# Kernel tuning notes

Hardware: AMD Instinct MI355X
Metric: run time of the kernel (lower is better)

Reference implementation:

```python
import jax, jax.numpy as jnp
import numpy as np

B, S, H, NH, HD, ROT = 4, 1024, 2048, 16, 128, 64
P = NH * HD  # attention projection size = 2048
EPS = 1e-6


def setup_inputs() -> dict:
    key = jax.random.key(0)
    ks = jax.random.split(key, 12)
    T = B * S
    # rotary frequency table [max_pos=S, 1, ROT]
    inv_freq = 1.0 / (10000.0 ** (np.arange(0, ROT, 2, dtype=np.float32) / ROT))
    f = np.outer(np.arange(S, dtype=np.float32), inv_freq)  # [S, ROT/2]
    freqs = np.concatenate([f, f], axis=-1)[:, None, :].astype(np.float32)
    sc = 0.02
    return {
        "positions": jnp.tile(jnp.arange(S, dtype=jnp.int64), B),  # per-seq positions 0..S-1
        "hidden_states": jax.random.normal(ks[0], (T, H), jnp.float32),
        "rotary_pos_emb": jnp.asarray(freqs),
        "lf1_cache": jax.random.normal(ks[1], (B, 1, H), jnp.float32) * sc,
        "lf2_cache": jax.random.normal(ks[2], (B, 1, H // 2), jnp.float32) * sc,
        "Wqk": jax.random.normal(ks[3], (2 * P, H), jnp.float32) * sc,
        "Wv": jax.random.normal(ks[4], (P, H), jnp.float32) * sc,
        "Wo": jax.random.normal(ks[5], (H, P), jnp.float32) * sc,
        "conv1_w": jax.random.normal(ks[6], (H // 2, H, 2), jnp.float32) * sc,  # [out, in, tap]
        "conv1_b": jnp.zeros((H // 2,), jnp.float32),
        "conv2_w": jax.random.normal(ks[7], (H, H // 2, 2), jnp.float32) * sc,
        "conv2_b": jnp.zeros((H,), jnp.float32),
        "ln_g": jnp.ones((H,), jnp.float32),
    }


def reference(positions, hidden_states, rotary_pos_emb, lf1_cache, lf2_cache,
              Wqk, Wv, Wo, conv1_w, conv1_b, conv2_w, conv2_b, ln_g):
    T = hidden_states.shape[0]
    scaling = HD ** -0.5

    # v projection on raw hidden states (done before lf_gate in the source)
    v = hidden_states @ Wv.T  # [T, P]

    # ---- LocalizedFiltering (two causal 2-tap convs + residual + RMSNorm),
    # vectorized over all sequences (source loops per sequence) ----
    x = hidden_states.reshape(B, S, H)
    xc = jnp.concatenate([lf1_cache, x], axis=1)  # [B, S+1, H]
    o1 = (jnp.einsum('bsh,oh->bso', xc[:, :-1], conv1_w[..., 0])
          + jnp.einsum('bsh,oh->bso', xc[:, 1:], conv1_w[..., 1]) + conv1_b)  # [B,S,H/2]
    o1c = jnp.concatenate([lf2_cache, o1], axis=1)  # [B, S+1, H/2]
    o2 = (jnp.einsum('bsc,oc->bso', o1c[:, :-1], conv2_w[..., 0])
          + jnp.einsum('bsc,oc->bso', o1c[:, 1:], conv2_w[..., 1]) + conv2_b)  # [B,S,H]
    o3 = o2 + x
    lf = o3 * jax.lax.rsqrt(jnp.mean(o3 * o3, axis=-1, keepdims=True) + EPS) * ln_g

    hs = lf.reshape(T, H)
    qk = (hs @ Wqk.T).reshape(T, NH, 2 * HD)
    q, k = jnp.split(qk, 2, axis=-1)  # each [T, NH, HD]

    # partial rotary (mscale = 1.0 since use_yarn=False)
    f = rotary_pos_emb[positions]            # [T, 1, ROT]
    cos, sin = jnp.cos(f), jnp.sin(f)

    def rope(t):
        tr, tp = t[..., :ROT], t[..., ROT:]
        t1, t2 = jnp.split(tr, 2, axis=-1)
        rot = jnp.concatenate([-t2, t1], axis=-1)
        return jnp.concatenate([tr * cos + rot * sin, tp], axis=-1)

    qb = rope(q).reshape(B, S, NH, HD)
    kb = rope(k).reshape(B, S, NH, HD)
    vb = v.reshape(B, S, NH, HD)

    # causal attention per sequence
    scores = jnp.einsum('bqhd,bkhd->bhqk', qb, kb) * scaling
    mask = jnp.tril(jnp.ones((S, S), bool))
    scores = jnp.where(mask, scores, jnp.finfo(scores.dtype).min)
    attn = jax.nn.softmax(scores, axis=-1)
    out = jnp.einsum('bhqk,bkhd->bqhd', attn, vb).reshape(T, P)
    return out @ Wo.T  # [T, H]
```

## Files before the change

### kernel.cpp

```cpp
#include <hip/hip_runtime.h>

typedef __bf16 bf16;
typedef __bf16 bf16x8 __attribute__((ext_vector_type(8)));
typedef __bf16 bf16x4 __attribute__((ext_vector_type(4)));
typedef float f32x4 __attribute__((ext_vector_type(4)));

#define DEVI __device__ __forceinline__

constexpr int Bc = 4, Sc = 1024, Hc = 2048, NHc = 16, HDc = 128;
constexpr int Tc = Bc * Sc;
constexpr int Pc = NHc * HDc;

DEVI void async16(const void* g, void* l) {
  __builtin_amdgcn_global_load_lds(
      (const __attribute__((address_space(1))) unsigned int*)g,
      (__attribute__((address_space(3))) unsigned int*)l, 16, 0, 0);
}

#define BAR() __builtin_amdgcn_s_barrier()
#define LGKM0()                                          \
  do {                                                   \
    asm volatile("s_waitcnt lgkmcnt(0)" ::: "memory");   \
    __builtin_amdgcn_sched_barrier(0);                   \
  } while (0)
#define VM0() asm volatile("s_waitcnt vmcnt(0)" ::: "memory")

template <int WM, int WN, int MREP, int NREP, bool OUT_BF16>
__global__ __launch_bounds__(512, 2) void gemm8(
    const bf16* __restrict__ A, const bf16* __restrict__ W, void* __restrict__ Cout,
    const float* __restrict__ bias, int M, int N, int K) {
  constexpr int BM = WM * MREP * 16;
  constexpr int BN = WN * NREP * 16;
  constexpr int MH = MREP / 2, NH = NREP / 2;
  constexpr int LA = BM / 128;
  constexpr int LB = BN / 128;
  constexpr int STG = (BM + BN) * 128;
  constexpr int OUTB = OUT_BF16 ? 2 : 4;
  constexpr int CBYTES = BM * BN * OUTB;
  constexpr int LDSB = (2 * STG > CBYTES) ? 2 * STG : CBYTES;
  __shared__ char lds[LDSB];

  const int nbx = N / BN;
  const int nwg = (M / BM) * nbx;
  const int wgid = (blockIdx.x & 7) * (nwg >> 3) + (blockIdx.x >> 3);
  const int bx = wgid % nbx, by = wgid / nbx;
  const int m0 = by * BM, n0 = bx * BN;
  const int tid = threadIdx.x;
  const int w = tid >> 6, l = tid & 63;
  const int wm = w / WN, wn = w % WN;
  const int lr = l & 15, hi = l >> 4;

  auto stageA = [&](int buf, int t, int half) {
#pragma unroll
    for (int c = 0; c < LA; ++c) {
      const int ch = c * 512 + tid;
      const int row = half * (BM / 2) + (ch >> 3);
      const int grp = ch & 7;
      async16(A + (size_t)(m0 + row) * K + (t << 6) + ((grp ^ (row & 7)) << 3),
              &lds[buf * STG + row * 128 + grp * 16]);
    }
  };
  auto stageB = [&](int buf, int t, int half) {
#pragma unroll
    for (int c = 0; c < LB; ++c) {
      const int ch = c * 512 + tid;
      const int row = half * (BN / 2) + (ch >> 3);
      const int grp = ch & 7;
      async16(W + (size_t)(n0 + row) * K + (t << 6) + ((grp ^ (row & 7)) << 3),
              &lds[buf * STG + BM * 128 + row * 128 + grp * 16]);
    }
  };
  auto LD = [&](const char* Lp, int row, int g) -> bf16x8 {
    return *(const bf16x8*)(Lp + ((size_t)row << 7) + ((g ^ (row & 7)) << 4));
  };

#define QUAD(MB_, NB_, FB_)                                                     \
  do {                                                                          \
    __builtin_amdgcn_s_setprio(1);                                              \
    _Pragma("unroll") for (int m = 0; m < MH; ++m)                              \
      _Pragma("unroll") for (int n = 0; n < NH; ++n)                            \
        _Pragma("unroll") for (int kk = 0; kk < 2; ++kk)                        \
          acc[(MB_) + m][(NB_) + n] = __builtin_amdgcn_mfma_f32_16x16x32_bf16(  \
              fa[m][kk], FB_[n][kk], acc[(MB_) + m][(NB_) + n], 0, 0, 0);       \
    __builtin_amdgcn_s_setprio(0);                                              \
  } while (0)

  f32x4 acc[MREP][NREP] = {};
  bf16x8 fa[MH][2], fb0[NH][2], fb1[NH][2];
  const int nk = K >> 6;

  stageA(0, 0, 0);
  stageB(0, 0, 0);
  stageB(0, 0, 1);
  stageA(0, 0, 1);
  VM0();
  BAR();

#pragma unroll 1
  for (int t = 0; t < nk; ++t) {
    const char* Lb = &lds[(t & 1) * STG];
    const int nbuf = (t & 1) ^ 1;
    const bool pf = (t + 1 < nk);
#pragma unroll
    for (int m = 0; m < MH; ++m) {
      const int r = wm * (MREP * 16) + m * 16 + lr;
      fa[m][0] = LD(Lb, r, hi);
      fa[m][1] = LD(Lb, r, 4 + hi);
    }
#pragma unroll
    for (int n = 0; n < NH; ++n) {
      const int r = BM + wn * (NREP * 16) + n * 16 + lr;
      fb0[n][0] = LD(Lb, r, hi);
      fb0[n][1] = LD(Lb, r, 4 + hi);
    }
    if (pf) {
      stageA(nbuf, t + 1, 0);
      stageB(nbuf, t + 1, 0);
    }
    BAR();
    LGKM0();
    QUAD(0, 0, fb0);
    BAR();
#pragma unroll
    for (int n = 0; n < NH; ++n) {
      const int r = BM + wn * (NREP * 16) + (NH + n) * 16 + lr;
      fb1[n][0] = LD(Lb, r, hi);
      fb1[n][1] = LD(Lb, r, 4 + hi);
    }
    if (pf) {
      stageB(nbuf, t + 1, 1);
      stageA(nbuf, t + 1, 1);
    }
    BAR();
    LGKM0();
    QUAD(0, NH, fb1);
    BAR();
#pragma unroll
    for (int m = 0; m < MH; ++m) {
      const int r = wm * (MREP * 16) + (MH + m) * 16 + lr;
      fa[m][0] = LD(Lb, r, hi);
      fa[m][1] = LD(Lb, r, 4 + hi);
    }
    BAR();
    LGKM0();
    QUAD(MH, NH, fb1);
    BAR();
    QUAD(MH, 0, fb0);
    VM0();
    BAR();
  }
#undef QUAD

  if constexpr (OUT_BF16) {
    bf16* cl = (bf16*)lds;
#pragma unroll
    for (int mi = 0; mi < MREP; ++mi) {
#pragma unroll
      for (int ni = 0; ni < NREP; ++ni) {
        const int col = wn * (NREP * 16) + ni * 16 + lr;
        const float bv = bias ? bias[n0 + col] : 0.f;
#pragma unroll
        for (int j = 0; j < 4; ++j) {
          const int row = wm * (MREP * 16) + mi * 16 + (hi << 2) + j;
          cl[row * BN + ((((col >> 3) ^ (row & 7)) << 3) | (col & 7))] =
              (bf16)(acc[mi][ni][j] + bv);
        }
      }
    }
    __syncthreads();
    constexpr int GPR = BN / 8;
    constexpr int PT = BM * GPR / 512;
#pragma unroll
    for (int c = 0; c < PT; ++c) {
      const int ch = c * 512 + tid;
      const int row = ch / GPR, g = ch % GPR;
      bf16x8 vv = *(const bf16x8*)&cl[row * BN + ((g ^ (row & 7)) << 3)];
      *(bf16x8*)&((bf16*)Cout)[(size_t)(m0 + row) * N + n0 + g * 8] = vv;
    }
  } else {
    float* cl = (float*)lds;
#pragma unroll
    for (int mi = 0; mi < MREP; ++mi) {
#pragma unroll
      for (int ni = 0; ni < NREP; ++ni) {
        const int col = wn * (NREP * 16) + ni * 16 + lr;
        const float bv = bias ? bias[n0 + col] : 0.f;
#pragma unroll
        for (int j = 0; j < 4; ++j) {
          const int row = wm * (MREP * 16) + mi * 16 + (hi << 2) + j;
          cl[row * BN + ((((col >> 2) ^ (row & 7)) << 2) | (col & 3))] =
              acc[mi][ni][j] + bv;
        }
      }
    }
    __syncthreads();
    constexpr int GPR = BN / 4;
    constexpr int PT = BM * GPR / 512;
#pragma unroll
    for (int c = 0; c < PT; ++c) {
      const int ch = c * 512 + tid;
      const int row = ch / GPR, g = ch % GPR;
      f32x4 vv = *(const f32x4*)&cl[row * BN + ((g ^ (row & 7)) << 2)];
      *(f32x4*)&((float*)Cout)[(size_t)(m0 + row) * N + n0 + g * 4] = vv;
    }
  }
}

template <int WM, int WN, int MREP, int NREP, bool OUT_BF16>
__global__ __launch_bounds__(WM * WN * 64, 2) void gemm_pipe(
    const bf16* __restrict__ A, const bf16* __restrict__ W, void* __restrict__ Cout,
    const float* __restrict__ bias, int M, int N, int K) {
  constexpr int BM = WM * MREP * 16;
  constexpr int BN = WN * NREP * 16;
  constexpr int THREADS = WM * WN * 64;
  constexpr int ROWS = BM + BN;
  constexpr int CHA = BM * 4 / THREADS;
  constexpr int CHB = BN * 4 / THREADS;
  static_assert(CHA + CHB == 4, "vmcnt ledger assumes 4 loads/thread/stage");
  __shared__ bf16 lds[4][ROWS * 32];
  static_assert(BM * BN * 2 <= sizeof(lds), "C tile must fit LDS for epilogue");

  const int nbx = N / BN;
  const int nwg = (M / BM) * nbx;
  const int wgid = (blockIdx.x & 7) * (nwg >> 3) + (blockIdx.x >> 3);
  const int bx = wgid % nbx, by = wgid / nbx;
  const int m0 = by * BM, n0 = bx * BN;
  const int tid = threadIdx.x;
  const int w = tid >> 6, l = tid & 63;
  const int wm = w / WN, wn = w % WN;
  const int lr = l & 15;
  const int hi = l >> 4;

  auto stage = [&](int slot, int t) {
    const int k0 = t << 5;
#pragma unroll
    for (int c = 0; c < CHA; ++c) {
      const int ch = c * THREADS + tid;
      const int row = ch >> 2, cg = ch & 3;
      const int gc = (cg ^ ((row >> 1) & 3)) << 3;
      async16(A + (size_t)(m0 + row) * K + k0 + gc, (char*)&lds[slot][0] + ch * 16);
    }
#pragma unroll
    for (int c = 0; c < CHB; ++c) {
      const int ch = c * THREADS + tid;
      const int row = ch >> 2, cg = ch & 3;
      const int gc = (cg ^ ((row >> 1) & 3)) << 3;
      async16(W + (size_t)(n0 + row) * K + k0 + gc,
              (char*)&lds[slot][0] + (BM * 4 + ch) * 16);
    }
  };

  f32x4 acc[MREP][NREP] = {};
  const int nk = K >> 5;

  stage(0, 0);
  stage(1, 1);
  stage(2, 2);
  asm volatile("s_waitcnt vmcnt(8)" ::: "memory");
  __builtin_amdgcn_s_barrier();
  __builtin_amdgcn_sched_barrier(0);

  bf16x8 fAc[MREP], fBc[NREP], fAn[MREP], fBn[NREP];
  {
    const char* nb = (const char*)&lds[0][0];
#pragma unroll
    for (int mi = 0; mi < MREP; ++mi) {
      const int r = wm * (MREP * 16) + mi * 16 + lr;
      fAc[mi] = *(const bf16x8*)(nb + r * 64 + ((hi ^ ((r >> 1) & 3)) << 4));
    }
#pragma unroll
    for (int ni = 0; ni < NREP; ++ni) {
      const int r = BM + wn * (NREP * 16) + ni * 16 + lr;
      fBc[ni] = *(const bf16x8*)(nb + r * 64 + ((hi ^ ((r >> 1) & 3)) << 4));
    }
  }

#define GSTEP(T_, CA, CB, NA, NB)                                              \
  do {                                                                         \
    if ((T_) + 2 < nk) asm volatile("s_waitcnt vmcnt(4)" ::: "memory");        \
    else               asm volatile("s_waitcnt vmcnt(0)" ::: "memory");        \
    __builtin_amdgcn_s_barrier();                                              \
    __builtin_amdgcn_sched_barrier(0);                                         \
    if ((T_) + 3 < nk) stage(((T_) + 3) & 3, (T_) + 3);                        \
    if ((T_) + 1 < nk) {                                                       \
      const char* nb = (const char*)&lds[((T_) + 1) & 3][0];                   \
      _Pragma("unroll") for (int mi = 0; mi < MREP; ++mi) {                    \
        const int r = wm * (MREP * 16) + mi * 16 + lr;                         \
        NA[mi] = *(const bf16x8*)(nb + r * 64 + ((hi ^ ((r >> 1) & 3)) << 4)); \
      }                                                                        \
      _Pragma("unroll") for (int ni = 0; ni < NREP; ++ni) {                    \
        const int r = BM + wn * (NREP * 16) + ni * 16 + lr;                    \
        NB[ni] = *(const bf16x8*)(nb + r * 64 + ((hi ^ ((r >> 1) & 3)) << 4)); \
      }                                                                        \
    }                                                                          \
    __builtin_amdgcn_s_setprio(1);                                             \
    _Pragma("unroll") for (int mi = 0; mi < MREP; ++mi)                        \
      _Pragma("unroll") for (int ni = 0; ni < NREP; ++ni)                      \
        acc[mi][ni] =                                                          \
            __builtin_amdgcn_mfma_f32_16x16x32_bf16(CA[mi], CB[ni], acc[mi][ni], 0, 0, 0); \
    __builtin_amdgcn_s_setprio(0);                                             \
  } while (0)

  for (int t = 0; t < nk; t += 2) {
    GSTEP(t, fAc, fBc, fAn, fBn);
    GSTEP(t + 1, fAn, fBn, fAc, fBc);
  }
#undef GSTEP

  __syncthreads();
  {
    bf16* cl = (bf16*)&lds[0][0];
#pragma unroll
    for (int mi = 0; mi < MREP; ++mi) {
#pragma unroll
      for (int ni = 0; ni < NREP; ++ni) {
        const int col = wn * (NREP * 16) + ni * 16 + lr;
        const float bv = bias ? bias[n0 + col] : 0.f;
#pragma unroll
        for (int j = 0; j < 4; ++j) {
          const int row = wm * (MREP * 16) + mi * 16 + (hi << 2) + j;
          cl[row * BN + ((((col >> 3) ^ (row & 7)) << 3) | (col & 7))] =
              (bf16)(acc[mi][ni][j] + bv);
        }
      }
    }
    __syncthreads();
    constexpr int GPR = BN / 8;
    constexpr int PT = BM * GPR / THREADS;
#pragma unroll
    for (int c = 0; c < PT; ++c) {
      const int ch = c * THREADS + tid;
      const int row = ch / GPR, g = ch % GPR;
      bf16x8 vv = *(const bf16x8*)&cl[row * BN + ((g ^ (row & 7)) << 3)];
      *(bf16x8*)&((bf16*)Cout)[(size_t)(m0 + row) * N + n0 + g * 8] = vv;
    }
  }
}

__global__ void k_f2b4(const float* __restrict__ in, bf16* __restrict__ out, int n4) {
  int i = blockIdx.x * 256 + threadIdx.x;
  if (i >= n4) return;
  float4 v = ((const float4*)in)[i];
  bf16x4 o = {(bf16)v.x, (bf16)v.y, (bf16)v.z, (bf16)v.w};
  ((bf16x4*)out)[i] = o;
}

__global__ void k_build_a1(const float* __restrict__ hid, const float* __restrict__ lf1,
                           bf16* __restrict__ hsb, bf16* __restrict__ A1) {
  int idx = blockIdx.x * 256 + threadIdx.x;
  int t = idx >> 11, h = idx & 2047;
  float x = hid[idx];
  hsb[idx] = (bf16)x;
  float xp;
  if ((t & (Sc - 1)) == 0)
    xp = lf1[(t >> 10) * Hc + h];
  else
    xp = hid[idx - Hc];
  size_t a = ((size_t)t << 12) + 2 * h;
  A1[a] = (bf16)xp;
  A1[a + 1] = (bf16)x;
}

__global__ void k_build_a2(const bf16* __restrict__ o1, const float* __restrict__ lf2,
                           bf16* __restrict__ A2) {
  int idx = blockIdx.x * 256 + threadIdx.x;
  int t = idx >> 10, c = idx & 1023;
  bf16 cur = o1[idx];
  bf16 prev;
  if ((t & (Sc - 1)) == 0)
    prev = (bf16)lf2[(t >> 10) * 1024 + c];
  else
    prev = o1[idx - 1024];
  size_t a = ((size_t)t << 11) + 2 * c;
  A2[a] = prev;
  A2[a + 1] = cur;
}

__global__ __launch_bounds__(256) void k_rmsnorm(const bf16* __restrict__ o2,
                                                 const float* __restrict__ hid,
                                                 const float* __restrict__ g,
                                                 bf16* __restrict__ lf) {
  int t = blockIdx.x, tid = threadIdx.x;
  size_t base = ((size_t)t << 11) + tid * 8;
  bf16x8 ov = *(const bf16x8*)&o2[base];
  const float* hp = &hid[base];
  float vals[8];
  float ss = 0.f;
#pragma unroll
  for (int i = 0; i < 8; ++i) {
    float x = (float)ov[i] + hp[i];
    vals[i] = x;
    ss += x * x;
  }
#pragma unroll
  for (int off = 1; off < 64; off <<= 1) ss += __shfl_xor(ss, off);
  __shared__ float red[4];
  if ((tid & 63) == 0) red[tid >> 6] = ss;
  __syncthreads();
  float tot = red[0] + red[1] + red[2] + red[3];
  float inv = rsqrtf(tot * (1.f / 2048.f) + 1e-6f);
  bf16x8 o;
#pragma unroll
  for (int i = 0; i < 8; ++i) o[i] = (bf16)(vals[i] * inv * g[tid * 8 + i]);
  *(bf16x8*)&lf[base] = o;
}

__global__ void k_rope(const bf16* __restrict__ qk, const float* __restrict__ rot,
                       bf16* __restrict__ qr, bf16* __restrict__ kr) {
  int bid = blockIdx.x;
  int n = bid & 15, t = bid >> 4;
  int s = t & (Sc - 1), b = t >> 10;
  int tid = threadIdx.x;
  int isk = tid >> 7, d = tid & 127;
  const bf16* src = qk + ((size_t)t << 12) + n * 256 + isk * 128;
  float val = (float)src[d];
  float outv = val;
  if (d < 64) {
    float f = rot[s * 64 + d];
    float c = cosf(f), sn = sinf(f);
    float other = (float)src[d ^ 32];
    outv = (d < 32) ? (val * c - other * sn) : (val * c + other * sn);
  }
  bf16* dst = isk ? kr : qr;
  dst[((size_t)((b * 16 + n) * 1024 + s) << 7) + d] = (bf16)outv;
}

__global__ void k_vt(const bf16* __restrict__ v, bf16* __restrict__ vT) {
  __shared__ bf16 tile[32][33];
  int bid = blockIdx.x;
  int dt = bid & 3;
  int st = (bid >> 2) & 31;
  int bn = bid >> 7;
  int b = bn >> 4, n = bn & 15;
  int tx = threadIdx.x & 31, ty = threadIdx.x >> 5;
#pragma unroll
  for (int i = 0; i < 4; ++i) {
    int s = st * 32 + ty + i * 8;
    int d = dt * 32 + tx;
    tile[ty + i * 8][tx] = v[(size_t)(b * 1024 + s) * 2048 + n * 128 + d];
  }
  __syncthreads();
#pragma unroll
  for (int i = 0; i < 4; ++i) {
    int d = dt * 32 + ty + i * 8;
    int s = st * 32 + tx;
    vT[((size_t)(bn * 128 + d)) * 1024 + s] = tile[tx][ty + i * 8];
  }
}

__global__ __launch_bounds__(256, 2) void k_attn(const bf16* __restrict__ qr,
                                                 const bf16* __restrict__ kr,
                                                 const bf16* __restrict__ vT,
                                                 bf16* __restrict__ att) {
  __shared__ bf16 Ks[2][64 * 128];
  __shared__ bf16 Vs[2][128 * 64];
  __shared__ bf16 plds[4][16 * 64];
  const int bid = blockIdx.x;
  const int xcd = bid & 7, jj = bid >> 3;
  const int bn = xcd * 8 + (jj >> 3);
  const int pr = jj & 7;
  const int tid = threadIdx.x, w = tid >> 6, l = tid & 63;
  const int lr = l & 15, hi = l >> 4;
  const bf16* kb = kr + ((size_t)bn << 17);
  const bf16* vb = vT + ((size_t)bn << 17);
  const int b = bn >> 4, hh = bn & 15;
  const float scaling = 0.08838834764831845f;

  auto stage = [&](int buf, int kt) {
#pragma unroll
    for (int c = 0; c < 4; ++c) {
      int chunk = c * 256 + tid;
      int prow = chunk >> 4, pcg = chunk & 15;
      async16(kb + ((size_t)(kt * 64 + prow) << 7) + ((pcg ^ (prow & 7)) << 3),
              (char*)&Ks[buf][0] + chunk * 16);
    }
#pragma unroll
    for (int c = 0; c < 4; ++c) {
      int chunk = c * 256 + tid;
      int prow = chunk >> 3, pcg = chunk & 7;
      async16(vb + ((size_t)prow << 10) + kt * 64 + ((pcg ^ (prow & 7)) << 3),
              (char*)&Vs[buf][0] + chunk * 16);
    }
  };

#pragma unroll 1
  for (int phase = 0; phase < 2; ++phase) {
    const int qt = phase ? (15 - pr) : pr;
    const int qg0 = qt * 64 + w * 16;
    const bf16* qb = qr + ((size_t)(bn * 1024 + qg0) << 7);
    bf16x8 qf[4];
#pragma unroll
    for (int ks = 0; ks < 4; ++ks) qf[ks] = *(const bf16x8*)&qb[lr * 128 + ks * 32 + hi * 8];
    f32x4 oacc[8] = {};
    float mrow[4] = {-1e30f, -1e30f, -1e30f, -1e30f};
    float lrow[4] = {0.f, 0.f, 0.f, 0.f};
    const int nkb = qt + 1;

    stage(0, 0);
    __syncthreads();

    for (int kbt = 0; kbt < nkb; ++kbt) {
      const int cur = kbt & 1;
      if (kbt + 1 < nkb) stage(cur ^ 1, kbt + 1);

      f32x4 sacc[4] = {};
#pragma unroll
      for (int n = 0; n < 4; ++n) {
        const int krow = n * 16 + lr;
#pragma unroll
        for (int ks = 0; ks < 4; ++ks) {
          bf16x8 kf = *(const bf16x8*)&Ks[cur][(krow << 7) + ((((ks << 2) | hi) ^ (krow & 7)) << 3)];
          sacc[n] = __builtin_amdgcn_mfma_f32_16x16x32_bf16(qf[ks], kf, sacc[n], 0, 0, 0);
        }
      }
      const bool needmask = (kbt * 64 + 63 > qg0);
#pragma unroll
      for (int n = 0; n < 4; ++n) {
        int kg = kbt * 64 + n * 16 + lr;
#pragma unroll
        for (int j = 0; j < 4; ++j) {
          float sv = sacc[n][j] * scaling;
          if (needmask && kg > qg0 + hi * 4 + j) sv = -1e30f;
          sacc[n][j] = sv;
        }
      }
      float sf[4];
#pragma unroll
      for (int j = 0; j < 4; ++j) {
        float pm = fmaxf(fmaxf(sacc[0][j], sacc[1][j]), fmaxf(sacc[2][j], sacc[3][j]));
        pm = fmaxf(pm, __shfl_xor(pm, 1));
        pm = fmaxf(pm, __shfl_xor(pm, 2));
        pm = fmaxf(pm, __shfl_xor(pm, 4));
        pm = fmaxf(pm, __shfl_xor(pm, 8));
        float mn = fmaxf(mrow[j], pm);
        sf[j] = __expf(mrow[j] - mn);
        mrow[j] = mn;
      }
#pragma unroll
      for (int n = 0; n < 4; ++n)
#pragma unroll
        for (int j = 0; j < 4; ++j) sacc[n][j] = __expf(sacc[n][j] - mrow[j]);
#pragma unroll
      for (int j = 0; j < 4; ++j) {
        float ps = sacc[0][j] + sacc[1][j] + sacc[2][j] + sacc[3][j];
        ps += __shfl_xor(ps, 1);
        ps += __shfl_xor(ps, 2);
        ps += __shfl_xor(ps, 4);
        ps += __shfl_xor(ps, 8);
        lrow[j] = lrow[j] * sf[j] + ps;
      }
#pragma unroll
      for (int dt = 0; dt < 8; ++dt)
#pragma unroll
        for (int j = 0; j < 4; ++j) oacc[dt][j] *= sf[j];
#pragma unroll
      for (int n = 0; n < 4; ++n)
#pragma unroll
        for (int j = 0; j < 4; ++j)
          plds[w][(hi * 4 + j) * 64 + n * 16 + lr] = (bf16)sacc[n][j];
      asm volatile("s_waitcnt lgkmcnt(0)" ::: "memory");
#pragma unroll
      for (int ks2 = 0; ks2 < 2; ++ks2) {
        bf16x8 pf = *(const bf16x8*)&plds[w][lr * 64 + ks2 * 32 + hi * 8];
#pragma unroll
        for (int dt = 0; dt < 8; ++dt) {
          const int vrow = dt * 16 + lr;
          bf16x8 vf = *(const bf16x8*)&Vs[cur][(vrow << 6) + ((((ks2 << 2) | hi) ^ (lr & 7)) << 3)];
          oacc[dt] = __builtin_amdgcn_mfma_f32_16x16x32_bf16(pf, vf, oacc[dt], 0, 0, 0);
        }
      }
      __syncthreads();
    }

#pragma unroll
    for (int j = 0; j < 4; ++j) {
      float inv = 1.f / lrow[j];
      int qg = qg0 + hi * 4 + j;
      size_t obase = ((size_t)(b * 1024 + qg) << 11) + hh * 128;
#pragma unroll
      for (int dt = 0; dt < 8; ++dt) att[obase + dt * 16 + lr] = (bf16)(oacc[dt][j] * inv);
    }
  }
}

extern "C" void kernel_launch(void* const* d_in, const int* in_sizes, int n_in,
                              void* d_out, int out_size, void* d_ws, size_t ws_size,
                              hipStream_t stream) {
  const float* hid = (const float*)d_in[1];
  const float* rot = (const float*)d_in[2];
  const float* lf1 = (const float*)d_in[3];
  const float* lf2 = (const float*)d_in[4];
  const float* Wqk = (const float*)d_in[5];
  const float* Wv  = (const float*)d_in[6];
  const float* Wo  = (const float*)d_in[7];
  const float* c1w = (const float*)d_in[8];
  const float* c1b = (const float*)d_in[9];
  const float* c2w = (const float*)d_in[10];
  const float* c2b = (const float*)d_in[11];
  const float* lng = (const float*)d_in[12];
  float* outp = (float*)d_out;
  char* ws = (char*)d_ws;

  const size_t MB = 1ull << 20;
  bf16* Wslot = (bf16*)(ws + 0 * MB);
  bf16* A1    = (bf16*)(ws + 16 * MB);
  bf16* qkb   = A1;
  bf16* hsb   = (bf16*)(ws + 48 * MB);
  bf16* lfb   = hsb;
  bf16* vT    = hsb;
  bf16* v     = (bf16*)(ws + 64 * MB);
  bf16* att   = v;
  bf16* o1    = (bf16*)(ws + 80 * MB);
  bf16* A2    = (bf16*)(ws + 88 * MB);
  bf16* qr    = A2;
  bf16* o2    = (bf16*)(ws + 104 * MB);
  bf16* kr    = o2;

  auto f2b = [&](const float* in, bf16* out, int n) {
    int n4 = n / 4;
    k_f2b4<<<(n4 + 255) / 256, 256, 0, stream>>>(in, out, n4);
  };

  f2b(Wv, Wslot, 2048 * 2048);
  k_build_a1<<<Tc * Hc / 256, 256, 0, stream>>>(hid, lf1, hsb, A1);
  gemm8<4, 2, 4, 4, true><<<256, 512, 0, stream>>>(hsb, Wslot, v, nullptr, Tc, Pc, Hc);

  f2b(c1w, Wslot, 1024 * 2048 * 2);
  gemm_pipe<2, 2, 4, 4, true><<<256, 256, 0, stream>>>(A1, Wslot, o1, c1b, Tc, 1024, 4096);

  k_build_a2<<<Tc * 1024 / 256, 256, 0, stream>>>(o1, lf2, A2);
  f2b(c2w, Wslot, 2048 * 1024 * 2);
  gemm8<4, 2, 4, 4, true><<<256, 512, 0, stream>>>(A2, Wslot, o2, c2b, Tc, 2048, 2048);

  k_rmsnorm<<<Tc, 256, 0, stream>>>(o2, hid, lng, lfb);

  f2b(Wqk, Wslot, 4096 * 2048);
  gemm8<2, 4, 8, 4, true><<<256, 512, 0, stream>>>(lfb, Wslot, qkb, nullptr, Tc, 4096, Hc);

  k_rope<<<Tc * NHc, 256, 0, stream>>>(qkb, rot, qr, kr);
  k_vt<<<64 * 32 * 4, 256, 0, stream>>>(v, vT);
  k_attn<<<Bc * NHc * 8, 256, 0, stream>>>(qr, kr, vT, att);

  f2b(Wo, Wslot, 2048 * 2048);
  gemm8<4, 2, 4, 4, false><<<256, 512, 0, stream>>>(att, Wslot, outp, nullptr, Tc, 2048, 2048);
}
```

Measured before the change: 389.9 us.

## Fuse RoPE and V-transpose into GEMM epilogues, drop separate kernels

The QK projection GEMM now applies partial rotary embedding in its epilogue and writes q and k directly in head-major layout. The V projection GEMM writes its tile transposed straight into the vT layout. This removes the separate k_rope and k_vt kernels along with their extra global read and write passes over qk and v, and two launches. In exchange the epilogues compute sin and cos per element and issue strided stores, and the workspace buffers are reassigned.

```diff
diff --git a/kernel.cpp b/kernel.cpp
--- a/kernel.cpp
+++ b/kernel.cpp
@@ -25,17 +25,19 @@
   } while (0)
 #define VM0() asm volatile("s_waitcnt vmcnt(0)" ::: "memory")
 
-template <int WM, int WN, int MREP, int NREP, bool OUT_BF16>
+template <int WM, int WN, int MREP, int NREP, int EPI>
 __global__ __launch_bounds__(512, 2) void gemm8(
-    const bf16* __restrict__ A, const bf16* __restrict__ W, void* __restrict__ Cout,
-    const float* __restrict__ bias, int M, int N, int K) {
+    const bf16* __restrict__ A, const bf16* __restrict__ W,
+    void* __restrict__ C0, void* __restrict__ C1,
+    const float* __restrict__ biasf, const float* __restrict__ rotf,
+    int M, int N, int K) {
   constexpr int BM = WM * MREP * 16;
   constexpr int BN = WN * NREP * 16;
   constexpr int MH = MREP / 2, NH = NREP / 2;
   constexpr int LA = BM / 128;
   constexpr int LB = BN / 128;
   constexpr int STG = (BM + BN) * 128;
-  constexpr int OUTB = OUT_BF16 ? 2 : 4;
+  constexpr int OUTB = (EPI == 3) ? 4 : 2;
   constexpr int CBYTES = BM * BN * OUTB;
   constexpr int LDSB = (2 * STG > CBYTES) ? 2 * STG : CBYTES;
   __shared__ char lds[LDSB];
@@ -151,14 +153,14 @@
   }
 #undef QUAD
 
-  if constexpr (OUT_BF16) {
+  if constexpr (EPI == 0) {
     bf16* cl = (bf16*)lds;
 #pragma unroll
-    for (int mi = 0; mi < MREP; ++mi) {
+    for (int mi = 0; mi < MREP; ++mi)
 #pragma unroll
       for (int ni = 0; ni < NREP; ++ni) {
         const int col = wn * (NREP * 16) + ni * 16 + lr;
-        const float bv = bias ? bias[n0 + col] : 0.f;
+        const float bv = biasf ? biasf[n0 + col] : 0.f;
 #pragma unroll
         for (int j = 0; j < 4; ++j) {
           const int row = wm * (MREP * 16) + mi * 16 + (hi << 2) + j;
@@ -166,7 +168,6 @@
               (bf16)(acc[mi][ni][j] + bv);
         }
       }
-    }
     __syncthreads();
     constexpr int GPR = BN / 8;
     constexpr int PT = BM * GPR / 512;
@@ -175,16 +176,88 @@
       const int ch = c * 512 + tid;
       const int row = ch / GPR, g = ch % GPR;
       bf16x8 vv = *(const bf16x8*)&cl[row * BN + ((g ^ (row & 7)) << 3)];
-      *(bf16x8*)&((bf16*)Cout)[(size_t)(m0 + row) * N + n0 + g * 8] = vv;
+      *(bf16x8*)&((bf16*)C0)[(size_t)(m0 + row) * N + n0 + g * 8] = vv;
+    }
+  } else if constexpr (EPI == 1) {
+    bf16* cl = (bf16*)lds;
+#pragma unroll
+    for (int mi = 0; mi < MREP; ++mi)
+#pragma unroll
+      for (int ni = 0; ni < NREP; ++ni) {
+        const int col = wn * (NREP * 16) + ni * 16 + lr;
+#pragma unroll
+        for (int j = 0; j < 4; ++j) {
+          const int row = wm * (MREP * 16) + mi * 16 + (hi << 2) + j;
+          cl[col * BM + ((((row >> 3) ^ (col & 7)) << 3) | (row & 7))] =
+              (bf16)acc[mi][ni][j];
+        }
+      }
+    __syncthreads();
+    const int s0 = m0 & 1023, bq = m0 >> 10;
+    bf16* vT = (bf16*)C0;
+    const size_t vbase = (((size_t)(bq * 16 + (n0 >> 7)) * 128) << 10) + s0;
+    constexpr int GPR = BM / 8;
+    constexpr int PT = BN * GPR / 512;
+#pragma unroll
+    for (int c = 0; c < PT; ++c) {
+      const int ch = c * 512 + tid;
+      const int d = ch / GPR, g = ch % GPR;
+      bf16x8 vv = *(const bf16x8*)&cl[d * BM + ((g ^ (d & 7)) << 3)];
+      *(bf16x8*)&vT[vbase + ((size_t)d << 10) + g * 8] = vv;
+    }
+  } else if constexpr (EPI == 2) {
+    bf16* cl = (bf16*)lds;
+#pragma unroll
+    for (int mi = 0; mi < MREP; ++mi)
+#pragma unroll
+      for (int ni = 0; ni < NREP; ++ni) {
+        const int col = wn * (NREP * 16) + ni * 16 + lr;
+#pragma unroll
+        for (int j = 0; j < 4; ++j) {
+          const int row = wm * (MREP * 16) + mi * 16 + (hi << 2) + j;
+          cl[row * BN + ((((col >> 3) ^ (row & 7)) << 3) | (col & 7))] =
+              (bf16)acc[mi][ni][j];
+        }
+      }
+    __syncthreads();
+    const int s0 = m0 & 1023, bq = m0 >> 10, head = n0 >> 8;
+    bf16* qr = (bf16*)C0;
+    bf16* kr = (bf16*)C1;
+    const size_t qbase = ((size_t)((bq * 16 + head) * 1024 + s0) << 7);
+    constexpr int GPR = BN / 8;
+    constexpr int PT = BM * GPR / 512;
+#pragma unroll
+    for (int c = 0; c < PT; ++c) {
+      const int ch = c * 512 + tid;
+      const int row = ch / GPR, g = ch % GPR;
+      const int cc = g * 8;
+      const int isk = cc >> 7, dd = cc & 127;
+      bf16x8 vv = *(const bf16x8*)&cl[row * BN + ((g ^ (row & 7)) << 3)];
+      bf16x8 out;
+      if (dd < 64) {
+        bf16x8 pp = *(const bf16x8*)&cl[row * BN + (((g ^ 4) ^ (row & 7)) << 3)];
+        const float* rp = &rotf[(s0 + row) * 64 + dd];
+#pragma unroll
+        for (int e = 0; e < 8; ++e) {
+          const float f = rp[e];
+          const float cf = cosf(f), sf = sinf(f);
+          const float pv = (dd < 32) ? -(float)pp[e] : (float)pp[e];
+          out[e] = (bf16)((float)vv[e] * cf + pv * sf);
+        }
+      } else {
+        out = vv;
+      }
+      bf16* dst = isk ? kr : qr;
+      *(bf16x8*)&dst[qbase + ((size_t)row << 7) + dd] = out;
     }
   } else {
     float* cl = (float*)lds;
 #pragma unroll
-    for (int mi = 0; mi < MREP; ++mi) {
+    for (int mi = 0; mi < MREP; ++mi)
 #pragma unroll
       for (int ni = 0; ni < NREP; ++ni) {
         const int col = wn * (NREP * 16) + ni * 16 + lr;
-        const float bv = bias ? bias[n0 + col] : 0.f;
+        const float bv = biasf ? biasf[n0 + col] : 0.f;
 #pragma unroll
         for (int j = 0; j < 4; ++j) {
           const int row = wm * (MREP * 16) + mi * 16 + (hi << 2) + j;
@@ -192,7 +265,6 @@
               acc[mi][ni][j] + bv;
         }
       }
-    }
     __syncthreads();
     constexpr int GPR = BN / 4;
     constexpr int PT = BM * GPR / 512;
@@ -201,12 +273,12 @@
       const int ch = c * 512 + tid;
       const int row = ch / GPR, g = ch % GPR;
       f32x4 vv = *(const f32x4*)&cl[row * BN + ((g ^ (row & 7)) << 2)];
-      *(f32x4*)&((float*)Cout)[(size_t)(m0 + row) * N + n0 + g * 4] = vv;
+      *(f32x4*)&((float*)C0)[(size_t)(m0 + row) * N + n0 + g * 4] = vv;
     }
   }
 }
 
-template <int WM, int WN, int MREP, int NREP, bool OUT_BF16>
+template <int WM, int WN, int MREP, int NREP>
 __global__ __launch_bounds__(WM * WN * 64, 2) void gemm_pipe(
     const bf16* __restrict__ A, const bf16* __restrict__ W, void* __restrict__ Cout,
     const float* __restrict__ bias, int M, int N, int K) {
@@ -405,49 +477,6 @@
   *(bf16x8*)&lf[base] = o;
 }
 
-__global__ void k_rope(const bf16* __restrict__ qk, const float* __restrict__ rot,
-                       bf16* __restrict__ qr, bf16* __restrict__ kr) {
-  int bid = blockIdx.x;
-  int n = bid & 15, t = bid >> 4;
-  int s = t & (Sc - 1), b = t >> 10;
-  int tid = threadIdx.x;
-  int isk = tid >> 7, d = tid & 127;
-  const bf16* src = qk + ((size_t)t << 12) + n * 256 + isk * 128;
-  float val = (float)src[d];
-  float outv = val;
-  if (d < 64) {
-    float f = rot[s * 64 + d];
-    float c = cosf(f), sn = sinf(f);
-    float other = (float)src[d ^ 32];
-    outv = (d < 32) ? (val * c - other * sn) : (val * c + other * sn);
-  }
-  bf16* dst = isk ? kr : qr;
-  dst[((size_t)((b * 16 + n) * 1024 + s) << 7) + d] = (bf16)outv;
-}
-
-__global__ void k_vt(const bf16* __restrict__ v, bf16* __restrict__ vT) {
-  __shared__ bf16 tile[32][33];
-  int bid = blockIdx.x;
-  int dt = bid & 3;
-  int st = (bid >> 2) & 31;
-  int bn = bid >> 7;
-  int b = bn >> 4, n = bn & 15;
-  int tx = threadIdx.x & 31, ty = threadIdx.x >> 5;
-#pragma unroll
-  for (int i = 0; i < 4; ++i) {
-    int s = st * 32 + ty + i * 8;
-    int d = dt * 32 + tx;
-    tile[ty + i * 8][tx] = v[(size_t)(b * 1024 + s) * 2048 + n * 128 + d];
-  }
-  __syncthreads();
-#pragma unroll
-  for (int i = 0; i < 4; ++i) {
-    int d = dt * 32 + ty + i * 8;
-    int s = st * 32 + tx;
-    vT[((size_t)(bn * 128 + d)) * 1024 + s] = tile[tx][ty + i * 8];
-  }
-}
-
 __global__ __launch_bounds__(256, 2) void k_attn(const bf16* __restrict__ qr,
                                                  const bf16* __restrict__ kr,
                                                  const bf16* __restrict__ vT,
@@ -604,17 +633,15 @@
   const size_t MB = 1ull << 20;
   bf16* Wslot = (bf16*)(ws + 0 * MB);
   bf16* A1    = (bf16*)(ws + 16 * MB);
-  bf16* qkb   = A1;
+  bf16* qr    = (bf16*)(ws + 16 * MB);
+  bf16* kr    = (bf16*)(ws + 32 * MB);
   bf16* hsb   = (bf16*)(ws + 48 * MB);
   bf16* lfb   = hsb;
-  bf16* vT    = hsb;
-  bf16* v     = (bf16*)(ws + 64 * MB);
-  bf16* att   = v;
+  bf16* vT    = (bf16*)(ws + 64 * MB);
   bf16* o1    = (bf16*)(ws + 80 * MB);
   bf16* A2    = (bf16*)(ws + 88 * MB);
-  bf16* qr    = A2;
+  bf16* att   = A2;
   bf16* o2    = (bf16*)(ws + 104 * MB);
-  bf16* kr    = o2;
 
   auto f2b = [&](const float* in, bf16* out, int n) {
     int n4 = n / 4;
@@ -623,24 +650,26 @@
 
   f2b(Wv, Wslot, 2048 * 2048);
   k_build_a1<<<Tc * Hc / 256, 256, 0, stream>>>(hid, lf1, hsb, A1);
-  gemm8<4, 2, 4, 4, true><<<256, 512, 0, stream>>>(hsb, Wslot, v, nullptr, Tc, Pc, Hc);
+  gemm8<4, 2, 4, 4, 1><<<256, 512, 0, stream>>>(hsb, Wslot, vT, nullptr, nullptr, nullptr,
+                                                Tc, Pc, Hc);
 
   f2b(c1w, Wslot, 1024 * 2048 * 2);
-  gemm_pipe<2, 2, 4, 4, true><<<256, 256, 0, stream>>>(A1, Wslot, o1, c1b, Tc, 1024, 4096);
+  gemm_pipe<2, 2, 4, 4><<<256, 256, 0, stream>>>(A1, Wslot, o1, c1b, Tc, 1024, 4096);
 
   k_build_a2<<<Tc * 1024 / 256, 256, 0, stream>>>(o1, lf2, A2);
   f2b(c2w, Wslot, 2048 * 1024 * 2);
-  gemm8<4, 2, 4, 4, true><<<256, 512, 0, stream>>>(A2, Wslot, o2, c2b, Tc, 2048, 2048);
+  gemm8<4, 2, 4, 4, 0><<<256, 512, 0, stream>>>(A2, Wslot, o2, nullptr, c2b, nullptr,
+                                                Tc, 2048, 2048);
 
   k_rmsnorm<<<Tc, 256, 0, stream>>>(o2, hid, lng, lfb);
 
   f2b(Wqk, Wslot, 4096 * 2048);
-  gemm8<2, 4, 8, 4, true><<<256, 512, 0, stream>>>(lfb, Wslot, qkb, nullptr, Tc, 4096, Hc);
-
-  k_rope<<<Tc * NHc, 256, 0, stream>>>(qkb, rot, qr, kr);
-  k_vt<<<64 * 32 * 4, 256, 0, stream>>>(v, vT);
+  gemm8<2, 4, 8, 4, 2><<<256, 512, 0, stream>>>(lfb, Wslot, qr, kr, nullptr, rot,
+                                                Tc, 4096, Hc);
+
   k_attn<<<Bc * NHc * 8, 256, 0, stream>>>(qr, kr, vT, att);
 
   f2b(Wo, Wslot, 2048 * 2048);
-  gemm8<4, 2, 4, 4, false><<<256, 512, 0, stream>>>(att, Wslot, outp, nullptr, Tc, 2048, 2048);
-}
+  gemm8<4, 2, 4, 4, 3><<<256, 512, 0, stream>>>(att, Wslot, outp, nullptr, nullptr, nullptr,
+                                                Tc, 2048, 2048);
+}
```

Result: slower. 431.8 us (+10.8%).
